# Kernel optimization log

Measured on AMD Instinct MI355X. Metric: run time of the kernel, lower is better.

Reference implementation:

```python
import jax, jax.numpy as jnp
import numpy as np

B, S, D = 64, 2048, 512

def setup_inputs() -> dict:
    key = jax.random.key(0)
    k1, k2, k3, k4, k5, k6 = jax.random.split(key, 6)
    hidden2 = jax.random.normal(k1, (B, D), dtype=jnp.float32)
    enc_key = jax.random.normal(k2, (B, S, D), dtype=jnp.float32)
    enc_value = jax.random.normal(k3, (B, S, D), dtype=jnp.float32)
    seq_lens = jax.random.randint(k4, (B,), 1, S + 1)  # valid lengths in [1, S]
    W = jax.random.normal(k5, (D, D), dtype=jnp.float32) / np.sqrt(D)
    b = jax.random.normal(k6, (D,), dtype=jnp.float32) * 0.01
    return {"hidden2": hidden2, "key": enc_key, "value": enc_value,
            "seq_lens": seq_lens, "W": W, "b": b}

def reference(hidden2, key, value, seq_lens, W, b):
    # query = Linear(hidden2): [B, D]
    query = hidden2 @ W.T + b
    # scores E = bmm(key, query): [B, S]
    E = jnp.einsum('bsd,bd->bs', key, query)
    # per-sample padding mask: positions >= seq_lens[i] get -inf
    mask = jnp.arange(S)[None, :] < seq_lens[:, None]  # [B, S]
    E = jnp.where(mask, E, -jnp.inf)
    attn = jax.nn.softmax(E, axis=-1)  # [B, S]
    context = jnp.einsum('bs,bsd->bd', attn, value)  # [B, D]
    return (context, attn[:, None, :])  # attn reshaped to [B, 1, S] as in torch
```

## Files before the change

### kernel.cpp

```cpp
#include <hip/hip_runtime.h>
#include <math.h>

#define BB 64
#define SS 2048
#define DD 512

__global__ void query_kernel(const float* __restrict__ hidden2,
                             const float* __restrict__ W,
                             const float* __restrict__ bias,
                             float* __restrict__ q) {
    const int b    = blockIdx.y;
    const int wave = threadIdx.x >> 6;
    const int lane = threadIdx.x & 63;
    const int d    = blockIdx.x * 4 + wave;

    const float4* h4 = reinterpret_cast<const float4*>(hidden2 + (size_t)b * DD);
    const float4* w4 = reinterpret_cast<const float4*>(W + (size_t)d * DD);
    float4 a0 = h4[lane];
    float4 a1 = h4[64 + lane];
    float4 b0 = w4[lane];
    float4 b1 = w4[64 + lane];
    float p = a0.x*b0.x + a0.y*b0.y + a0.z*b0.z + a0.w*b0.w
            + a1.x*b1.x + a1.y*b1.y + a1.z*b1.z + a1.w*b1.w;
    #pragma unroll
    for (int off = 32; off; off >>= 1) p += __shfl_xor(p, off, 64);
    if (lane == 0) q[b * DD + d] = p + bias[d];
}

__global__ void scores_kernel(const float* __restrict__ key,
                              const float* __restrict__ q,
                              const int* __restrict__ seq_lens,
                              float* __restrict__ E) {
    const int b   = blockIdx.y;
    const int len = seq_lens[b];
    const int s0  = blockIdx.x * 16;
    if (s0 >= len) return;

    const int wave = threadIdx.x >> 6;
    const int lane = threadIdx.x & 63;

    const float4* q4 = reinterpret_cast<const float4*>(q + (size_t)b * DD);
    const float4 q0 = q4[lane];
    const float4 q1 = q4[64 + lane];

    #pragma unroll
    for (int r = 0; r < 4; ++r) {
        const int s = s0 + wave * 4 + r;
        if (s >= len) break;
        const float4* k4 =
            reinterpret_cast<const float4*>(key + ((size_t)b * SS + s) * DD);
        float4 k0 = k4[lane];
        float4 k1 = k4[64 + lane];
        float p = k0.x*q0.x + k0.y*q0.y + k0.z*q0.z + k0.w*q0.w
                + k1.x*q1.x + k1.y*q1.y + k1.z*q1.z + k1.w*q1.w;
        #pragma unroll
        for (int off = 32; off; off >>= 1) p += __shfl_xor(p, off, 64);
        if (lane == 0) E[b * SS + s] = p;
    }
}

__global__ void softmax_kernel(const float* __restrict__ E,
                               const int* __restrict__ seq_lens,
                               float* __restrict__ attn,
                               float* __restrict__ ctx) {
    const int b = blockIdx.x;
    const int t = threadIdx.x;

    if (t < DD / 4)
        reinterpret_cast<float4*>(ctx + (size_t)b * DD)[t] = make_float4(0, 0, 0, 0);

    const int len = seq_lens[b];
    const float* e = E + (size_t)b * SS;
    float* a = attn + (size_t)b * SS;

    __shared__ float red[256];

    float m = -INFINITY;
    for (int s = t; s < len; s += 256) m = fmaxf(m, e[s]);
    red[t] = m; __syncthreads();
    #pragma unroll
    for (int off = 128; off; off >>= 1) {
        if (t < off) red[t] = fmaxf(red[t], red[t + off]);
        __syncthreads();
    }
    m = red[0];
    __syncthreads();

    float sum = 0.f;
    for (int s = t; s < len; s += 256) {
        float p = __expf(e[s] - m);
        a[s] = p;
        sum += p;
    }
    red[t] = sum; __syncthreads();
    #pragma unroll
    for (int off = 128; off; off >>= 1) {
        if (t < off) red[t] += red[t + off];
        __syncthreads();
    }
    const float inv = 1.0f / red[0];

    for (int s = t; s < len; s += 256) a[s] *= inv;
    for (int s = len + t; s < SS; s += 256) a[s] = 0.f;
}

__global__ void context_kernel(const float* __restrict__ value,
                               const float* __restrict__ attn,
                               const int* __restrict__ seq_lens,
                               float* __restrict__ ctx) {
    const int b   = blockIdx.y;
    const int len = seq_lens[b];
    const int s0  = blockIdx.x * 64;
    if (s0 >= len) return;
    const int send = min(s0 + 64, len);
    const int t = threadIdx.x;

    __shared__ float as[64];
    if (t < 64) as[t] = attn[(size_t)b * SS + s0 + t];
    __syncthreads();

    float acc = 0.f;
    const float* v = value + ((size_t)b * SS + s0) * DD + t;
    for (int s = s0; s < send; ++s, v += DD)
        acc += as[s - s0] * (*v);

    atomicAdd(&ctx[b * DD + t], acc);
}

extern "C" void kernel_launch(void* const* d_in, const int* in_sizes, int n_in,
                              void* d_out, int out_size, void* d_ws, size_t ws_size,
                              hipStream_t stream) {
    const float* hidden2  = (const float*)d_in[0];
    const float* key      = (const float*)d_in[1];
    const float* value    = (const float*)d_in[2];
    const int*   seq_lens = (const int*)  d_in[3];
    const float* W        = (const float*)d_in[4];
    const float* bias     = (const float*)d_in[5];

    float* out  = (float*)d_out;
    float* ctx  = out;
    float* attn = out + BB * DD;

    float* ws = (float*)d_ws;
    float* q  = ws;
    float* E  = ws + BB * DD;

    query_kernel  <<<dim3(DD / 4, BB), 256, 0, stream>>>(hidden2, W, bias, q);
    scores_kernel <<<dim3(SS / 16, BB), 256, 0, stream>>>(key, q, seq_lens, E);
    softmax_kernel<<<BB, 256, 0, stream>>>(E, seq_lens, attn, ctx);
    context_kernel<<<dim3(SS / 64, BB), 512, 0, stream>>>(value, attn, seq_lens, ctx);
}
```

Baseline: 522.0 us.

## Fuse scores, softmax and context into split-softmax chunk kernel with combine pass

Replaces the separate scores, softmax and context kernels with one chunked kernel. It computes scores for 64 keys, a local max and sum, unnormalized attention, and a partial context over the matching value rows. A small combine kernel then rescales the per-chunk partials with the global max and sum, writes the final context, and normalizes attention. This removes the E round trip, the single-block-per-batch softmax stage and the atomics, at the cost of partial-context workspace traffic and an extra rescale pass over attention.

Result: faster. 491.5 us (-5.8%).

```diff
diff --git a/kernel.cpp b/kernel.cpp
--- a/kernel.cpp
+++ b/kernel.cpp
@@ -4,6 +4,8 @@
 #define BB 64
 #define SS 2048
 #define DD 512
+#define SC 64
+#define NC (SS / SC)
 
 __global__ void query_kernel(const float* __restrict__ hidden2,
                              const float* __restrict__ W,
@@ -27,104 +29,147 @@
     if (lane == 0) q[b * DD + d] = p + bias[d];
 }
 
-__global__ void scores_kernel(const float* __restrict__ key,
-                              const float* __restrict__ q,
-                              const int* __restrict__ seq_lens,
-                              float* __restrict__ E) {
-    const int b   = blockIdx.y;
-    const int len = seq_lens[b];
-    const int s0  = blockIdx.x * 16;
+__global__ void chunk_kernel(const float* __restrict__ key,
+                             const float* __restrict__ value,
+                             const float* __restrict__ q,
+                             const int* __restrict__ seq_lens,
+                             float* __restrict__ attn,
+                             float* __restrict__ mc,
+                             float* __restrict__ lc,
+                             float* __restrict__ ctxp) {
+    const int b     = blockIdx.y;
+    const int chunk = blockIdx.x;
+    const int len   = seq_lens[b];
+    const int s0    = chunk * SC;
     if (s0 >= len) return;
-
-    const int wave = threadIdx.x >> 6;
-    const int lane = threadIdx.x & 63;
+    const int nv = min(SC, len - s0);
+
+    const int t    = threadIdx.x;
+    const int wave = t >> 6;
+    const int lane = t & 63;
+
+    __shared__ float E_lds[SC];
+    __shared__ float p_lds[SC];
+    __shared__ float red[256];
+    __shared__ float4 cred[128];
 
     const float4* q4 = reinterpret_cast<const float4*>(q + (size_t)b * DD);
     const float4 q0 = q4[lane];
     const float4 q1 = q4[64 + lane];
 
-    #pragma unroll
-    for (int r = 0; r < 4; ++r) {
-        const int s = s0 + wave * 4 + r;
-        if (s >= len) break;
+    for (int r = wave; r < nv; r += 4) {
         const float4* k4 =
-            reinterpret_cast<const float4*>(key + ((size_t)b * SS + s) * DD);
+            reinterpret_cast<const float4*>(key + ((size_t)b * SS + s0 + r) * DD);
         float4 k0 = k4[lane];
         float4 k1 = k4[64 + lane];
         float p = k0.x*q0.x + k0.y*q0.y + k0.z*q0.z + k0.w*q0.w
                 + k1.x*q1.x + k1.y*q1.y + k1.z*q1.z + k1.w*q1.w;
         #pragma unroll
         for (int off = 32; off; off >>= 1) p += __shfl_xor(p, off, 64);
-        if (lane == 0) E[b * SS + s] = p;
-    }
-}
-
-__global__ void softmax_kernel(const float* __restrict__ E,
-                               const int* __restrict__ seq_lens,
-                               float* __restrict__ attn,
-                               float* __restrict__ ctx) {
-    const int b = blockIdx.x;
-    const int t = threadIdx.x;
-
-    if (t < DD / 4)
-        reinterpret_cast<float4*>(ctx + (size_t)b * DD)[t] = make_float4(0, 0, 0, 0);
-
-    const int len = seq_lens[b];
-    const float* e = E + (size_t)b * SS;
-    float* a = attn + (size_t)b * SS;
-
-    __shared__ float red[256];
-
-    float m = -INFINITY;
-    for (int s = t; s < len; s += 256) m = fmaxf(m, e[s]);
-    red[t] = m; __syncthreads();
+        if (lane == 0) E_lds[r] = p;
+    }
+    __syncthreads();
+
+    red[t] = (t < nv) ? E_lds[t] : -INFINITY;
+    __syncthreads();
     #pragma unroll
     for (int off = 128; off; off >>= 1) {
         if (t < off) red[t] = fmaxf(red[t], red[t + off]);
         __syncthreads();
     }
-    m = red[0];
-    __syncthreads();
-
-    float sum = 0.f;
-    for (int s = t; s < len; s += 256) {
-        float p = __expf(e[s] - m);
-        a[s] = p;
-        sum += p;
-    }
-    red[t] = sum; __syncthreads();
+    const float m_c = red[0];
+    __syncthreads();
+
+    float pv = 0.f;
+    if (t < nv) {
+        pv = __expf(E_lds[t] - m_c);
+        p_lds[t] = pv;
+        attn[(size_t)b * SS + s0 + t] = pv;
+    }
+    red[t] = pv;
+    __syncthreads();
     #pragma unroll
     for (int off = 128; off; off >>= 1) {
         if (t < off) red[t] += red[t + off];
         __syncthreads();
     }
-    const float inv = 1.0f / red[0];
-
-    for (int s = t; s < len; s += 256) a[s] *= inv;
-    for (int s = len + t; s < SS; s += 256) a[s] = 0.f;
-}
-
-__global__ void context_kernel(const float* __restrict__ value,
-                               const float* __restrict__ attn,
+    if (t == 0) {
+        mc[b * NC + chunk] = m_c;
+        lc[b * NC + chunk] = red[0];
+    }
+
+    const int d4   = t & 127;
+    const int half = t >> 7;
+    float4 acc = make_float4(0.f, 0.f, 0.f, 0.f);
+    for (int r = half; r < nv; r += 2) {
+        const float4 v = *reinterpret_cast<const float4*>(
+            value + ((size_t)b * SS + s0 + r) * DD + 4 * d4);
+        const float p = p_lds[r];
+        acc.x += p * v.x; acc.y += p * v.y; acc.z += p * v.z; acc.w += p * v.w;
+    }
+    __syncthreads();
+    if (half) cred[d4] = acc;
+    __syncthreads();
+    if (!half) {
+        const float4 o = cred[d4];
+        acc.x += o.x; acc.y += o.y; acc.z += o.z; acc.w += o.w;
+        *reinterpret_cast<float4*>(ctxp + ((size_t)b * NC + chunk) * DD + 4 * d4) = acc;
+    }
+}
+
+__global__ void combine_kernel(const float* __restrict__ mc,
+                               const float* __restrict__ lc,
+                               const float* __restrict__ ctxp,
                                const int* __restrict__ seq_lens,
+                               float* __restrict__ attn,
                                float* __restrict__ ctx) {
-    const int b   = blockIdx.y;
+    const int b   = blockIdx.x;
+    const int t   = threadIdx.x;
     const int len = seq_lens[b];
-    const int s0  = blockIdx.x * 64;
-    if (s0 >= len) return;
-    const int send = min(s0 + 64, len);
-    const int t = threadIdx.x;
-
-    __shared__ float as[64];
-    if (t < 64) as[t] = attn[(size_t)b * SS + s0 + t];
-    __syncthreads();
-
-    float acc = 0.f;
-    const float* v = value + ((size_t)b * SS + s0) * DD + t;
-    for (int s = s0; s < send; ++s, v += DD)
-        acc += as[s - s0] * (*v);
-
-    atomicAdd(&ctx[b * DD + t], acc);
+    const int ncb = (len + SC - 1) / SC;
+
+    __shared__ float sm[2];
+    __shared__ float sa[NC];
+    __shared__ float sc_[NC];
+
+    if (t < 64) {
+        const int lane = t;
+        float m_c = (lane < ncb) ? mc[b * NC + lane] : -INFINITY;
+        float l_c = (lane < ncb) ? lc[b * NC + lane] : 0.f;
+        float m = m_c;
+        #pragma unroll
+        for (int off = 32; off; off >>= 1) m = fmaxf(m, __shfl_xor(m, off, 64));
+        float le = l_c * __expf(m_c - m);
+        float l = le;
+        #pragma unroll
+        for (int off = 32; off; off >>= 1) l += __shfl_xor(l, off, 64);
+        if (lane == 0) { sm[0] = m; sm[1] = l; }
+        if (lane < NC) {
+            float e = (lane < ncb) ? __expf(m_c - m) : 0.f;
+            sc_[lane] = e;
+            sa[lane]  = e / l;
+        }
+    }
+    __syncthreads();
+    const float inv_l = 1.0f / sm[1];
+
+    if (t < 128) {
+        float4 acc = make_float4(0.f, 0.f, 0.f, 0.f);
+        for (int c = 0; c < ncb; ++c) {
+            const float4 v = *reinterpret_cast<const float4*>(
+                ctxp + ((size_t)b * NC + c) * DD + 4 * t);
+            const float s = sc_[c];
+            acc.x += s * v.x; acc.y += s * v.y; acc.z += s * v.z; acc.w += s * v.w;
+        }
+        acc.x *= inv_l; acc.y *= inv_l; acc.z *= inv_l; acc.w *= inv_l;
+        *reinterpret_cast<float4*>(ctx + (size_t)b * DD + 4 * t) = acc;
+    }
+
+    float* a = attn + (size_t)b * SS;
+    for (int s = t; s < SS; s += 256) {
+        if (s < len) a[s] *= sa[s >> 6];
+        else         a[s]  = 0.f;
+    }
 }
 
 extern "C" void kernel_launch(void* const* d_in, const int* in_sizes, int n_in,
@@ -141,12 +186,15 @@
     float* ctx  = out;
     float* attn = out + BB * DD;
 
-    float* ws = (float*)d_ws;
-    float* q  = ws;
-    float* E  = ws + BB * DD;
+    float* ws   = (float*)d_ws;
+    float* q    = ws;
+    float* mc   = ws + BB * DD;
+    float* lc   = mc + BB * NC;
+    float* ctxp = lc + BB * NC;
 
     query_kernel  <<<dim3(DD / 4, BB), 256, 0, stream>>>(hidden2, W, bias, q);
-    scores_kernel <<<dim3(SS / 16, BB), 256, 0, stream>>>(key, q, seq_lens, E);
-    softmax_kernel<<<BB, 256, 0, stream>>>(E, seq_lens, attn, ctx);
-    context_kernel<<<dim3(SS / 64, BB), 512, 0, stream>>>(value, attn, seq_lens, ctx);
-}
+    chunk_kernel  <<<dim3(NC, BB),     256, 0, stream>>>(key, value, q, seq_lens,
+                                                         attn, mc, lc, ctxp);
+    combine_kernel<<<BB,               256, 0, stream>>>(mc, lc, ctxp, seq_lens,
+                                                         attn, ctx);
+}
```
